# Kernel tuning notes

Measured on AMD Instinct MI355X. Metric: run time of the kernel, lower is better.

Reference implementation:

```python
import jax, jax.numpy as jnp
import numpy as np

BN_EPS = 1e-5

def _bn(x, gamma, beta, relu=True):
    # training-mode BatchNorm over all dims except channel (last)
    axes = tuple(range(x.ndim - 1))
    mu = jnp.mean(x, axes, keepdims=True)
    var = jnp.var(x, axes, keepdims=True)
    y = (x - mu) / jnp.sqrt(var + BN_EPS) * gamma + beta
    return jax.nn.relu(y) if relu else y

def _l2norm(x, eps):
    # F.normalize: x / max(||x||, eps)
    n = jnp.sqrt(jnp.sum(x * x, axis=-1, keepdims=True))
    return x / jnp.maximum(n, eps)

def setup_inputs() -> dict:
    key = jax.random.key(0)
    ks = jax.random.split(key, 16)
    B, N, H, W, C = 2, 512, 16, 32, 64
    IN_DIM = 10 + C + C + 2  # 140
    MLP3 = [128, 64]
    s = 0.02
    inp = {
        "warped_xyz": jax.random.normal(ks[0], (B, N, 3), jnp.float32),
        "warped_points": jax.random.normal(ks[1], (B, N, C), jnp.float32),
        "RF3": jax.random.normal(ks[2], (B, C, H, W), jnp.float32),
        "RF3_index": jax.random.normal(ks[3], (B, 3, H, W), jnp.float32),
        "lidar_z": jax.random.uniform(ks[4], (B, N, 1), jnp.float32),
        # conv1x1 stack (mlp3)
        "W1": jax.random.normal(ks[5], (IN_DIM, MLP3[0]), jnp.float32) * s,
        "b1": jnp.zeros((MLP3[0],), jnp.float32),
        "g1": jnp.ones((MLP3[0],), jnp.float32),
        "be1": jnp.zeros((MLP3[0],), jnp.float32),
        "W2": jax.random.normal(ks[6], (MLP3[0], MLP3[1]), jnp.float32) * s,
        "b2": jnp.zeros((MLP3[1],), jnp.float32),
        "g2": jnp.ones((MLP3[1],), jnp.float32),
        "be2": jnp.zeros((MLP3[1],), jnp.float32),
        # conv1d stack (mlp4 = [feats_dim//2], then 2 logits)
        "M1w": jax.random.normal(ks[7], (MLP3[1], MLP3[1] // 2), jnp.float32) * s,
        "M1b": jnp.zeros((MLP3[1] // 2,), jnp.float32),
        "M1g": jnp.ones((MLP3[1] // 2,), jnp.float32),
        "M1be": jnp.zeros((MLP3[1] // 2,), jnp.float32),
        "M2w": jax.random.normal(ks[8], (MLP3[1] // 2, 2), jnp.float32) * s,
        "M2b": jnp.zeros((2,), jnp.float32),
    }
    return inp

def reference(warped_xyz, warped_points, RF3, RF3_index, lidar_z,
              W1, b1, g1, be1, W2, b2, g2, be2,
              M1w, M1b, M1g, M1be, M2w, M2b):
    B, N, _ = warped_xyz.shape
    _, Ci, H, W_ = RF3.shape
    M = H * W_
    RF3_bnc = RF3.transpose(0, 2, 3, 1).reshape(B, M, Ci)          # [B,M,C]
    idx_bnc = RF3_index.transpose(0, 2, 3, 1).reshape(B, M, 3)     # [B,M,3]

    src_xyz = warped_xyz[:, :, None, :]                             # [B,N,1,3]
    dst_xyz = idx_bnc[:, None, :, :]                                # [B,1,M,3]
    euc = (src_xyz - dst_xyz)[..., :2]                              # [B,N,M,2]
    euc_norm = jnp.sqrt(euc[..., 0:1] ** 2 + euc[..., 1:2] ** 2)    # [B,N,M,1]

    xyz_z = (warped_xyz * lidar_z)[:, :, None, :]                   # [B,N,1,3]
    src_pts = warped_points[:, :, None, :]                          # [B,N,1,C]
    dst_pts = RF3_bnc[:, None, :, :]                                # [B,1,M,C]

    geom = jnp.concatenate([
        jnp.broadcast_to(xyz_z, (B, N, M, 3)),
        jnp.broadcast_to(src_pts[..., :2], (B, N, M, 2)),
        jnp.broadcast_to(dst_xyz[..., :2], (B, N, M, 2)),
        euc, euc_norm], axis=-1)                                    # [B,N,M,10]
    desc = jnp.concatenate([
        jnp.broadcast_to(src_pts, (B, N, M, Ci)),
        jnp.broadcast_to(dst_pts, (B, N, M, Ci))], axis=-1)         # [B,N,M,2C]

    # cal_sim: cosine sim between lidar feats (src) and image feats (dst)
    src_n = _l2norm(warped_points, 1e-12)
    dst_n = _l2norm(RF3_bnc, 1e-12)
    cos = jnp.einsum('bnc,bmc->bnm', src_n, dst_n)                  # [B,N,M]
    s1 = cos / (jnp.max(cos, axis=2, keepdims=True) + 1e-6)         # src->dst norm
    s2 = cos / (jnp.max(cos, axis=1, keepdims=True) + 1e-10)        # dst->src norm
    sim = jnp.stack([s1, s2], axis=-1)                              # [B,N,M,2]

    feats = jnp.concatenate([geom, desc, sim], axis=-1)             # [B,N,M,140]
    feats = _bn(jnp.einsum('bnmi,io->bnmo', feats, W1) + b1, g1, be1)
    feats = _bn(jnp.einsum('bnmi,io->bnmo', feats, W2) + b2, g2, be2)

    aw = jax.nn.softmax(jnp.max(feats, axis=-1), axis=-1)           # [B,N,M]
    att = jnp.einsum('bnm,bnmc->bnc', aw, feats)                    # [B,N,C]

    att = _bn(att @ M1w + M1b, M1g, M1be)
    logits = att @ M2w + M2b                                        # [B,N,2]
    return logits
```

## Files before the change

### kernel.cpp

```cpp
#include <hip/hip_runtime.h>
#include <hip/hip_bf16.h>

#define B_ 2
#define N_ 512
#define M_ 512
#define O1 128
#define O2 64
#define PBIG 524288.0f
#define P3   1024.0f

typedef short s8v __attribute__((ext_vector_type(8)));
typedef float f4v __attribute__((ext_vector_type(4)));

#define WS_SRCN 0
#define WS_DSTN 65536
#define WS_P0   0
#define WS_U    131072
#define WS_Z    131072
#define WS_V    262144
#define WS_DXY  393216
#define WS_COS  395264
#define WS_RMAX 919552
#define WS_ROWS 920576
#define WS_COLS 923648
#define WS_SC2P 935936
#define WS_ST2  936960
#define WS_ST3  945152
#define WS_CMAX 949248
#define WS_W2F  950272
#define WS_W9S  954368
#define WS_X2   961536
#define WS_VF   17738752

__device__ __forceinline__ unsigned short f2bf(float f){
  unsigned u = __float_as_uint(f);
  unsigned r = (u + 0x7fffu + ((u >> 16) & 1u)) >> 16;
  return (unsigned short)r;
}
__device__ __forceinline__ float bf2f(unsigned short h){
  return __uint_as_float(((unsigned)h) << 16);
}
__device__ __forceinline__ unsigned pk2(float lo, float hi){
  return (unsigned)f2bf(lo) | ((unsigned)f2bf(hi) << 16);
}
__device__ __forceinline__ unsigned pk_trunc(float lo, float hi){
  return __builtin_amdgcn_perm(__float_as_uint(hi), __float_as_uint(lo), 0x07060302u);
}
__device__ __forceinline__ f4v relu4(f4v z){
  z[0] = fmaxf(z[0], 0.f); z[1] = fmaxf(z[1], 0.f);
  z[2] = fmaxf(z[2], 0.f); z[3] = fmaxf(z[3], 0.f);
  return z;
}

__global__ __launch_bounds__(128) void k1(const float* __restrict__ wxyz,
    const float* __restrict__ wpts, const float* __restrict__ lz,
    const float* __restrict__ rf3, const float* __restrict__ rf3i,
    const float* __restrict__ W1, const float* __restrict__ W2, float* __restrict__ ws){
  int t = threadIdx.x;
  if (blockIdx.x < 1024){
    int blk = blockIdx.x; int b = blk >> 9, n = blk & 511;
    int bn = b*N_ + n;
    __shared__ float wp[64]; __shared__ float sxyz[3]; __shared__ float slz; __shared__ float srn;
    if (t < 64) wp[t] = wpts[bn*64 + t];
    if (t >= 64 && t < 67) sxyz[t-64] = wxyz[bn*3 + (t-64)];
    if (t == 67) slz = lz[bn];
    __syncthreads();
    if (t < 64){
      float v = wp[t]*wp[t];
      v += __shfl_down(v,32); v += __shfl_down(v,16); v += __shfl_down(v,8);
      v += __shfl_down(v,4);  v += __shfl_down(v,2);  v += __shfl_down(v,1);
      if (t == 0) srn = 1.0f / fmaxf(sqrtf(v), 1e-12f);
    }
    __syncthreads();
    if (t < 64) ws[WS_SRCN + bn*64 + t] = wp[t]*srn;
    int o = t;
    float x = sxyz[0], y = sxyz[1], z = sxyz[2], l = slz;
    float acc = x*l*W1[0*O1+o] + y*l*W1[1*O1+o] + z*l*W1[2*O1+o]
              + wp[0]*W1[3*O1+o] + wp[1]*W1[4*O1+o]
              + x*W1[7*O1+o] + y*W1[8*O1+o];
    #pragma unroll 8
    for (int c = 0; c < 64; ++c) acc += wp[c]*W1[(10+c)*O1+o];
    ws[WS_U + bn*O1 + o] = acc;
  } else if (blockIdx.x < 2048){
    int blk = blockIdx.x - 1024; int b = blk >> 9, m = blk & 511;
    int bm = b*M_ + m;
    __shared__ float rf[64]; __shared__ float sdx, sdy, srn2;
    if (t < 64) rf[t] = rf3[(b*64 + t)*512 + m];
    if (t == 64) sdx = rf3i[(b*3 + 0)*512 + m];
    if (t == 65) sdy = rf3i[(b*3 + 1)*512 + m];
    __syncthreads();
    if (t < 64){
      float v = rf[t]*rf[t];
      v += __shfl_down(v,32); v += __shfl_down(v,16); v += __shfl_down(v,8);
      v += __shfl_down(v,4);  v += __shfl_down(v,2);  v += __shfl_down(v,1);
      if (t == 0) srn2 = 1.0f / fmaxf(sqrtf(v), 1e-12f);
    }
    __syncthreads();
    if (t < 64) ws[WS_DSTN + bm*64 + t] = rf[t]*srn2;
    if (t == 0){ ws[WS_DXY + bm*2+0] = sdx; ws[WS_DXY + bm*2+1] = sdy; }
    int o = t;
    float acc = sdx*(W1[5*O1+o] - W1[7*O1+o]) + sdy*(W1[6*O1+o] - W1[8*O1+o]);
    #pragma unroll 8
    for (int c = 0; c < 64; ++c) acc += rf[c]*W1[(74+c)*O1+o];
    ws[WS_V + bm*O1 + o] = acc;
  } else {
    unsigned short* wf = (unsigned short*)(ws + WS_W2F);
    for (int i = t; i < 8192; i += 128){
      int j = i & 7, ll = (i >> 3) & 63, ct = (i >> 9) & 3, k0q = i >> 11;
      int oo = k0q*32 + (ll >> 4)*8 + j, c = ct*16 + (ll & 15);
      wf[i] = f2bf(W2[oo*O2 + c]);
    }
  }
}

__global__ __launch_bounds__(256) void k2(float* __restrict__ ws){
  int blk = blockIdx.x; int b = blk >> 9, n = blk & 511; int t = threadIdx.x;
  int bn = b*N_ + n;
  __shared__ __align__(16) float sn[64];
  __shared__ float dnt[64*65];
  __shared__ float part[4*64];
  if (t < 64) sn[t] = ws[WS_SRCN + bn*64 + t];
  float lmax = -3.4e38f;
  for (int chunk = 0; chunk < 8; ++chunk){
    __syncthreads();
    const float4* src = (const float4*)(ws + WS_DSTN + (size_t)(b*M_ + chunk*64)*64);
    #pragma unroll
    for (int i = 0; i < 4; ++i){
      float4 v = src[t + i*256];
      int base = (t + i*256)*4; int mm = base >> 6, c = base & 63;
      float* dp = &dnt[mm*65 + c];
      dp[0]=v.x; dp[1]=v.y; dp[2]=v.z; dp[3]=v.w;
    }
    __syncthreads();
    {
      int mm = t & 63, cg2 = t >> 6;
      const float* dr = &dnt[mm*65 + cg2*16];
      const float* sr = &sn[cg2*16];
      float p = 0.f;
      #pragma unroll
      for (int k = 0; k < 16; ++k) p += sr[k]*dr[k];
      part[cg2*64 + mm] = p;
    }
    __syncthreads();
    if (t < 64){
      float d = part[t] + part[64+t] + part[128+t] + part[192+t];
      ws[WS_COS + bn*M_ + chunk*64 + t] = d;
      lmax = fmaxf(lmax, d);
    }
  }
  if (t < 64){
    lmax = fmaxf(lmax, __shfl_xor(lmax,32)); lmax = fmaxf(lmax, __shfl_xor(lmax,16));
    lmax = fmaxf(lmax, __shfl_xor(lmax,8));  lmax = fmaxf(lmax, __shfl_xor(lmax,4));
    lmax = fmaxf(lmax, __shfl_xor(lmax,2));  lmax = fmaxf(lmax, __shfl_xor(lmax,1));
    if (t == 0) ws[WS_RMAX + bn] = 1.0f / (lmax + 1e-6f);
  }
}

__global__ __launch_bounds__(256) void k2r(const float* __restrict__ wxyz, float* __restrict__ ws){
  int blk = blockIdx.x;
  int b = blk >> 5; int c0 = (blk & 31)*16;
  int t = threadIdx.x;
  int cl = t & 15, seg = t >> 4;
  int col = c0 + cl;
  int bm = b*M_ + col;
  float dx = ws[WS_DXY + bm*2+0], dy = ws[WS_DXY + bm*2+1];
  float mx = -3.4e38f, se = 0.f, sc = 0.f, s1c = 0.f;
  for (int i = 0; i < 32; ++i){
    int bn = b*N_ + seg*32 + i;
    float cv = ws[WS_COS + (size_t)bn*M_ + col];
    float ri = ws[WS_RMAX + bn];
    float sx = wxyz[bn*3+0], sy = wxyz[bn*3+1];
    float ex = sx-dx, ey = sy-dy;
    se += sqrtf(ex*ex + ey*ey);
    mx = fmaxf(mx, cv);
    sc += cv;
    s1c += cv*ri;
  }
  __shared__ float r0[256], r1[256], r2[256], r3[256];
  r0[t]=mx; r1[t]=se; r2[t]=s1c; r3[t]=sc;
  __syncthreads();
  for (int s = 8; s > 0; s >>= 1){
    if (seg < s){
      int o2 = t + s*16;
      r0[t] = fmaxf(r0[t], r0[o2]); r1[t] += r1[o2]; r2[t] += r2[o2]; r3[t] += r3[o2];
    }
    __syncthreads();
  }
  if (t < 16){
    int bmw = b*M_ + c0 + t;
    float ci = 1.0f/(r0[t] + 1e-10f);
    ws[WS_CMAX + bmw] = ci;
    ws[WS_COLS + bmw] = r1[t];
    ws[WS_COLS + 1024 + bmw] = r2[t];
    ws[WS_COLS + 2048 + bmw] = r3[t]*ci;
  }
}

__global__ __launch_bounds__(256) void k3a(const float* __restrict__ wxyz, float* __restrict__ ws){
  int bn = blockIdx.x; int b = bn >> 9; int t = threadIdx.x;
  float ri = ws[WS_RMAX + bn];
  float sx = wxyz[bn*3+0], sy = wxyz[bn*3+1];
  float q[9];
  #pragma unroll
  for (int j = 0; j < 9; ++j) q[j] = 0.f;
  #pragma unroll
  for (int k = 0; k < 2; ++k){
    int m = t + k*256;
    float2 d = *(const float2*)(ws + WS_DXY + (size_t)(b*M_+m)*2);
    float ex = sx-d.x, ey = sy-d.y;
    float en = sqrtf(ex*ex + ey*ey);
    float cv = ws[WS_COS + (size_t)bn*M_ + m];
    float ci = ws[WS_CMAX + b*M_ + m];
    float s2 = cv*ci;
    q[0]+=en; q[1]+=cv; q[2]+=s2; q[3]+=en*en; q[4]+=cv*cv; q[5]+=s2*s2;
    q[6]+=en*cv; q[7]+=en*s2; q[8]+=cv*cv*ci;
  }
  #pragma unroll
  for (int j = 0; j < 9; ++j){
    float v = q[j];
    v += __shfl_xor(v,1); v += __shfl_xor(v,2); v += __shfl_xor(v,4);
    v += __shfl_xor(v,8); v += __shfl_xor(v,16); v += __shfl_xor(v,32);
    q[j] = v;
  }
  __shared__ float wr[9][4];
  int w = t >> 6;
  if ((t & 63) == 0){
    #pragma unroll
    for (int j = 0; j < 9; ++j) wr[j][w] = q[j];
  }
  __syncthreads();
  if (t < 9){
    float Q = wr[t][0] + wr[t][1] + wr[t][2] + wr[t][3];
    float f = (t==1 || t==6 || t==8) ? ri : ((t==4) ? ri*ri : 1.0f);
    float s = f*Q;
    if (t < 3) ws[WS_ROWS + t*1024 + bn] = s;
    atomicAdd(&ws[WS_SC2P + (bn & 63)*16 + t], s);
  }
}

__global__ __launch_bounds__(256) void k3s(const float* __restrict__ W1,
    const float* __restrict__ b1, const float* __restrict__ g1,
    const float* __restrict__ be1, float* __restrict__ ws){
  int o = blockIdx.x; int t = threadIdx.x;
  __shared__ float scal[9];
  __shared__ float wr[12][4];
  __shared__ float sA1, sC1;
  if (t < 9){
    float s = 0.f;
    #pragma unroll 8
    for (int r = 0; r < 64; ++r) s += ws[WS_SC2P + r*16 + t];
    scal[t] = s;
  }
  float b1o = b1[o];
  float uu[4], vv[4];
  float a[12];
  #pragma unroll
  for (int j = 0; j < 12; ++j) a[j] = 0.f;
  #pragma unroll
  for (int k = 0; k < 4; ++k){
    int i = t + k*256;
    float u = ws[WS_U + (size_t)i*O1 + o] + b1o;
    float v = ws[WS_V + (size_t)i*O1 + o];
    uu[k] = u; vv[k] = v;
    float ren = ws[WS_ROWS + i], rs1 = ws[WS_ROWS + 1024 + i], rs2 = ws[WS_ROWS + 2048 + i];
    float cen = ws[WS_COLS + i], cs1 = ws[WS_COLS + 1024 + i], cs2 = ws[WS_COLS + 2048 + i];
    a[0]+=u; a[1]+=u*u; a[2]+=u*ren; a[3]+=u*rs1; a[4]+=u*rs2;
    a[5]+=v; a[6]+=v*v; a[7]+=v*cen; a[8]+=v*cs1; a[9]+=v*cs2;
    if (k < 2){ a[10]+=u; a[11]+=v; }
  }
  #pragma unroll
  for (int j = 0; j < 12; ++j){
    float v = a[j];
    v += __shfl_xor(v,1); v += __shfl_xor(v,2); v += __shfl_xor(v,4);
    v += __shfl_xor(v,8); v += __shfl_xor(v,16); v += __shfl_xor(v,32);
    a[j] = v;
  }
  int w = t >> 6;
  if ((t & 63) == 0){
    #pragma unroll
    for (int j = 0; j < 12; ++j) wr[j][w] = a[j];
  }
  __syncthreads();
  if (t == 0){
    float A[12];
    #pragma unroll
    for (int j = 0; j < 12; ++j) A[j] = wr[j][0] + wr[j][1] + wr[j][2] + wr[j][3];
    float w9 = W1[9*O1+o], wa = W1[138*O1+o], wb = W1[139*O1+o];
    float S1 = 512.f*(A[0] + A[5]) + w9*scal[0] + wa*scal[1] + wb*scal[2];
    float Q1 = 512.f*(A[1] + A[6])
      + 2.f*(A[10]*A[11] + (A[0]-A[10])*(A[5]-A[11]))
      + w9*w9*scal[3] + wa*wa*scal[4] + wb*wb*scal[5]
      + 2.f*(w9*wa*scal[6] + w9*wb*scal[7] + wa*wb*scal[8])
      + 2.f*(w9*A[2] + wa*A[3] + wb*A[4])
      + 2.f*(w9*A[7] + wa*A[8] + wb*A[9]);
    float mu = S1/PBIG, var = Q1/PBIG - mu*mu;
    float istd = rsqrtf(var + 1e-5f);
    float A1v = g1[o]*istd;
    sA1 = A1v; sC1 = be1[o] - mu*A1v;
    ws[WS_W9S + o]       = w9*A1v;
    ws[WS_W9S + 128 + o] = wa*A1v;
    ws[WS_W9S + 256 + o] = wb*A1v;
  }
  __syncthreads();
  float A1 = sA1, C1 = sC1;
  int k0q = o >> 5, quad = (o >> 3) & 3, j = o & 7;
  #pragma unroll
  for (int k = 0; k < 4; ++k){
    int i = t + k*256;
    ws[WS_P0 + (size_t)i*O1 + o] = uu[k]*A1 + C1;
    int b = i >> 9, m = i & 511;
    int mc = m >> 7, w2 = (m >> 5) & 3, mt = (m >> 4) & 1, l16 = m & 15;
    ws[WS_VF + (size_t)(((b*4 + mc)*4 + w2)*4096) + k0q*1024 + mt*512 + (quad*16 + l16)*8 + j]
      = vv[k]*A1;
  }
}

__global__ __launch_bounds__(256, 4) void k4(const float* __restrict__ wxyz,
    float* __restrict__ ws){
  int blk = blockIdx.x; int bn = blk >> 2, mc = blk & 3;
  int b = bn >> 9; int t = threadIdx.x;
  __shared__ __align__(16) float p0s[128], w9s[128], was[128], wbs[128];
  __shared__ float ls[64], lq[64];
  if (t < 64){ ls[t] = 0.f; lq[t] = 0.f; }
  if (t < 128){
    p0s[t] = ws[WS_P0 + bn*O1 + t];
    w9s[t] = ws[WS_W9S + t];
    was[t] = ws[WS_W9S + 128 + t];
    wbs[t] = ws[WS_W9S + 256 + t];
  }
  __syncthreads();
  int ll = t & 63, w = t >> 6, l16 = ll & 15, quad = ll >> 4;
  float sx = wxyz[bn*3+0], sy = wxyz[bn*3+1];
  float ri = ws[WS_RMAX + bn];
  uint4* xf4 = (uint4*)(ws + WS_X2) + (size_t)bn*4096;
  const unsigned short* wBg = (const unsigned short*)(ws + WS_W2F);
  union U8 { s8v v; unsigned u[4]; };
  int mA = mc*128 + w*32 + l16, mB = mA + 16;
  float2 dA = *(const float2*)(ws + WS_DXY + (size_t)(b*M_+mA)*2);
  float2 dB = *(const float2*)(ws + WS_DXY + (size_t)(b*M_+mB)*2);
  float cvA = ws[WS_COS + (size_t)bn*M_ + mA], cvB = ws[WS_COS + (size_t)bn*M_ + mB];
  float ciA = ws[WS_CMAX + b*M_ + mA],         ciB = ws[WS_CMAX + b*M_ + mB];
  float exA = sx-dA.x, eyA = sy-dA.y; float en0 = sqrtf(exA*exA + eyA*eyA);
  float exB = sx-dB.x, eyB = sy-dB.y; float en1 = sqrtf(exB*exB + eyB*eyB);
  float s10 = cvA*ri, s20 = cvA*ciA;
  float s11 = cvB*ri, s21 = cvB*ciB;
  const float* vfb = ws + WS_VF + (size_t)(((b*4 + mc)*4 + w)*4096) + ll*8;
  f4v acc[2][4];
  #pragma unroll
  for (int i = 0; i < 2; ++i)
    #pragma unroll
    for (int j = 0; j < 4; ++j) acc[i][j] = (f4v){0.f,0.f,0.f,0.f};
  #pragma unroll
  for (int k0q = 0; k0q < 4; ++k0q){
    int ko = k0q*32 + quad*8;
    f4v p0a = *(const f4v*)&p0s[ko], p0b = *(const f4v*)&p0s[ko+4];
    f4v w9a = *(const f4v*)&w9s[ko], w9b = *(const f4v*)&w9s[ko+4];
    f4v waa = *(const f4v*)&was[ko], wab = *(const f4v*)&was[ko+4];
    f4v wba = *(const f4v*)&wbs[ko], wbb = *(const f4v*)&wbs[ko+4];
    const float* vA = vfb + k0q*1024;
    const float* vB = vA + 512;
    f4v vA0 = *(const f4v*)(vA), vA1 = *(const f4v*)(vA + 4);
    f4v vB0 = *(const f4v*)(vB), vB1 = *(const f4v*)(vB + 4);
    f4v zaA = relu4(p0a + vA0 + en0*w9a + s10*waa + s20*wba);
    f4v zbA = relu4(p0b + vA1 + en0*w9b + s10*wab + s20*wbb);
    f4v zaB = relu4(p0a + vB0 + en1*w9a + s11*waa + s21*wba);
    f4v zbB = relu4(p0b + vB1 + en1*w9b + s11*wab + s21*wbb);
    U8 uA, uB;
    uA.u[0] = pk_trunc(zaA[0], zaA[1]); uA.u[1] = pk_trunc(zaA[2], zaA[3]);
    uA.u[2] = pk_trunc(zbA[0], zbA[1]); uA.u[3] = pk_trunc(zbA[2], zbA[3]);
    uB.u[0] = pk_trunc(zaB[0], zaB[1]); uB.u[1] = pk_trunc(zaB[2], zaB[3]);
    uB.u[2] = pk_trunc(zbB[0], zbB[1]); uB.u[3] = pk_trunc(zbB[2], zbB[3]);
    #pragma unroll
    for (int ct = 0; ct < 4; ++ct){
      s8v bw = *(const s8v*)&wBg[((k0q*4 + ct)*64 + ll)*8];
      acc[0][ct] = __builtin_amdgcn_mfma_f32_16x16x32_bf16(bw, uA.v, acc[0][ct], 0,0,0);
      acc[1][ct] = __builtin_amdgcn_mfma_f32_16x16x32_bf16(bw, uB.v, acc[1][ct], 0,0,0);
    }
  }
  #pragma unroll
  for (int mt = 0; mt < 2; ++mt){
    uint4 u0, u1;
    u0.x = pk2(acc[mt][0][0], acc[mt][0][1]); u0.y = pk2(acc[mt][0][2], acc[mt][0][3]);
    u0.z = pk2(acc[mt][1][0], acc[mt][1][1]); u0.w = pk2(acc[mt][1][2], acc[mt][1][3]);
    u1.x = pk2(acc[mt][2][0], acc[mt][2][1]); u1.y = pk2(acc[mt][2][2], acc[mt][2][3]);
    u1.z = pk2(acc[mt][3][0], acc[mt][3][1]); u1.w = pk2(acc[mt][3][2], acc[mt][3][3]);
    xf4[((((mc*4 + w)*2 + mt)*2 + 0)*64) + ll] = u0;
    xf4[((((mc*4 + w)*2 + mt)*2 + 1)*64) + ll] = u1;
  }
  #pragma unroll
  for (int ct = 0; ct < 4; ++ct){
    #pragma unroll
    for (int r = 0; r < 4; ++r){
      float a0 = acc[0][ct][r], a1 = acc[1][ct][r];
      float s = a0 + a1;
      float q = a0*a0 + a1*a1;
      s += __shfl_xor(s,1); s += __shfl_xor(s,2); s += __shfl_xor(s,4); s += __shfl_xor(s,8);
      q += __shfl_xor(q,1); q += __shfl_xor(q,2); q += __shfl_xor(q,4); q += __shfl_xor(q,8);
      if (l16 == 0){
        atomicAdd(&ls[ct*16 + quad*4 + r], s);
        atomicAdd(&lq[ct*16 + quad*4 + r], q);
      }
    }
  }
  __syncthreads();
  int rep = blk & 63;
  if (t < 64) atomicAdd(&ws[WS_ST2 + rep*128 + t], ls[t]);
  else if (t < 128) atomicAdd(&ws[WS_ST2 + rep*128 + t], lq[t-64]);
}

__global__ __launch_bounds__(256) void k5(const float* __restrict__ g2,
    const float* __restrict__ be2, const float* __restrict__ M1w,
    const float* __restrict__ M1b, float* __restrict__ ws){
  int bn = blockIdx.x; int t = threadIdx.x;
  __shared__ float sa2[64], sc2[64];
  __shared__ float s_mx[512];
  __shared__ float s_aw[512];
  __shared__ float red[256];
  __shared__ float part[64*65];
  __shared__ float s_att[64];
  __shared__ float sgmax, sinvS;
  if (t < 64){
    float s = 0.f, q = 0.f;
    #pragma unroll 8
    for (int r = 0; r < 64; ++r){ s += ws[WS_ST2 + r*128 + t]; q += ws[WS_ST2 + r*128 + 64 + t]; }
    float mu = s/PBIG, var = q/PBIG - mu*mu;
    float istd = rsqrtf(var + 1e-5f);
    float A2 = g2[t]*istd;
    sa2[t] = A2; sc2[t] = be2[t] - mu*A2;
  }
  __syncthreads();
  int ll = t & 63, w = t >> 6, l16 = ll & 15, quad = ll >> 4;
  const uint4* xf4 = (const uint4*)(ws + WS_X2) + (size_t)bn*4096;
  uint4 xv[4][2][2];
  #pragma unroll
  for (int mc = 0; mc < 4; ++mc)
    #pragma unroll
    for (int mt = 0; mt < 2; ++mt)
      #pragma unroll
      for (int cp = 0; cp < 2; ++cp)
        xv[mc][mt][cp] = xf4[((((mc*4 + w)*2 + mt)*2 + cp)*64) + ll];
  float a2r[4][4], c2r[4][4];
  #pragma unroll
  for (int ct = 0; ct < 4; ++ct)
    #pragma unroll
    for (int r = 0; r < 4; ++r){
      int c = ct*16 + quad*4 + r;
      a2r[ct][r] = sa2[c]; c2r[ct][r] = sc2[c];
    }
  #pragma unroll
  for (int mc = 0; mc < 4; ++mc){
    #pragma unroll
    for (int mt = 0; mt < 2; ++mt){
      float mx = 0.f;
      #pragma unroll
      for (int cp = 0; cp < 2; ++cp){
        uint4 uv = xv[mc][mt][cp];
        int c0t = 2*cp, c1t = 2*cp + 1;
        float x0 = bf2f((unsigned short)(uv.x & 0xffffu));
        float x1 = bf2f((unsigned short)(uv.x >> 16));
        float x2 = bf2f((unsigned short)(uv.y & 0xffffu));
        float x3 = bf2f((unsigned short)(uv.y >> 16));
        float x4 = bf2f((unsigned short)(uv.z & 0xffffu));
        float x5 = bf2f((unsigned short)(uv.z >> 16));
        float x6 = bf2f((unsigned short)(uv.w & 0xffffu));
        float x7 = bf2f((unsigned short)(uv.w >> 16));
        mx = fmaxf(mx, a2r[c0t][0]*x0 + c2r[c0t][0]);
        mx = fmaxf(mx, a2r[c0t][1]*x1 + c2r[c0t][1]);
        mx = fmaxf(mx, a2r[c0t][2]*x2 + c2r[c0t][2]);
        mx = fmaxf(mx, a2r[c0t][3]*x3 + c2r[c0t][3]);
        mx = fmaxf(mx, a2r[c1t][0]*x4 + c2r[c1t][0]);
        mx = fmaxf(mx, a2r[c1t][1]*x5 + c2r[c1t][1]);
        mx = fmaxf(mx, a2r[c1t][2]*x6 + c2r[c1t][2]);
        mx = fmaxf(mx, a2r[c1t][3]*x7 + c2r[c1t][3]);
      }
      mx = fmaxf(mx, __shfl_xor(mx,16));
      mx = fmaxf(mx, __shfl_xor(mx,32));
      if (quad == 0) s_mx[mc*128 + w*32 + mt*16 + l16] = mx;
    }
  }
  __syncthreads();
  red[t] = fmaxf(s_mx[t], s_mx[t+256]);
  __syncthreads();
  for (int s = 128; s > 0; s >>= 1){ if (t < s) red[t] = fmaxf(red[t], red[t+s]); __syncthreads(); }
  if (t == 0) sgmax = red[0];
  __syncthreads();
  float e0 = expf(s_mx[t] - sgmax), e1 = expf(s_mx[t+256] - sgmax);
  s_aw[t] = e0; s_aw[t+256] = e1;
  red[t] = e0 + e1;
  __syncthreads();
  for (int s = 128; s > 0; s >>= 1){ if (t < s) red[t] += red[t+s]; __syncthreads(); }
  if (t == 0) sinvS = 1.0f / red[0];
  __syncthreads();
  float acc[4][4];
  #pragma unroll
  for (int ct = 0; ct < 4; ++ct)
    #pragma unroll
    for (int r = 0; r < 4; ++r) acc[ct][r] = 0.f;
  #pragma unroll
  for (int mc = 0; mc < 4; ++mc){
    #pragma unroll
    for (int mt = 0; mt < 2; ++mt){
      float aw = s_aw[mc*128 + w*32 + mt*16 + l16];
      #pragma unroll
      for (int cp = 0; cp < 2; ++cp){
        uint4 uv = xv[mc][mt][cp];
        int c0t = 2*cp, c1t = 2*cp + 1;
        float x0 = bf2f((unsigned short)(uv.x & 0xffffu));
        float x1 = bf2f((unsigned short)(uv.x >> 16));
        float x2 = bf2f((unsigned short)(uv.y & 0xffffu));
        float x3 = bf2f((unsigned short)(uv.y >> 16));
        float x4 = bf2f((unsigned short)(uv.z & 0xffffu));
        float x5 = bf2f((unsigned short)(uv.z >> 16));
        float x6 = bf2f((unsigned short)(uv.w & 0xffffu));
        float x7 = bf2f((unsigned short)(uv.w >> 16));
        acc[c0t][0] += aw*fmaxf(a2r[c0t][0]*x0 + c2r[c0t][0], 0.f);
        acc[c0t][1] += aw*fmaxf(a2r[c0t][1]*x1 + c2r[c0t][1], 0.f);
        acc[c0t][2] += aw*fmaxf(a2r[c0t][2]*x2 + c2r[c0t][2], 0.f);
        acc[c0t][3] += aw*fmaxf(a2r[c0t][3]*x3 + c2r[c0t][3], 0.f);
        acc[c1t][0] += aw*fmaxf(a2r[c1t][0]*x4 + c2r[c1t][0], 0.f);
        acc[c1t][1] += aw*fmaxf(a2r[c1t][1]*x5 + c2r[c1t][1], 0.f);
        acc[c1t][2] += aw*fmaxf(a2r[c1t][2]*x6 + c2r[c1t][2], 0.f);
        acc[c1t][3] += aw*fmaxf(a2r[c1t][3]*x7 + c2r[c1t][3], 0.f);
      }
    }
  }
  int row = w*16 + l16;
  #pragma unroll
  for (int ct = 0; ct < 4; ++ct)
    #pragma unroll
    for (int r = 0; r < 4; ++r)
      part[row*65 + ct*16 + quad*4 + r] = acc[ct][r];
  __syncthreads();
  if (t < 64){
    float a = 0.f;
    #pragma unroll 8
    for (int r = 0; r < 64; ++r) a += part[r*65 + t];
    s_att[t] = a * sinvS;
  }
  __syncthreads();
  if (t < 32){
    float z = M1b[t];
    #pragma unroll 8
    for (int c = 0; c < 64; ++c) z += s_att[c]*M1w[c*32 + t];
    ws[WS_Z + bn*32 + t] = z;
    int rep = bn & 63;
    atomicAdd(&ws[WS_ST3 + rep*64 + t], z);
    atomicAdd(&ws[WS_ST3 + rep*64 + 32 + t], z*z);
  }
}

__global__ __launch_bounds__(256) void k6(const float* __restrict__ M1g,
    const float* __restrict__ M1be, const float* __restrict__ M2w,
    const float* __restrict__ M2b, const float* __restrict__ ws, float* __restrict__ out){
  int t = threadIdx.x; int s = blockIdx.x*256 + t;
  __shared__ float sa3[32], sc3[32];
  if (t < 32){
    float su = 0.f, q = 0.f;
    #pragma unroll 8
    for (int r = 0; r < 64; ++r){ su += ws[WS_ST3 + r*64 + t]; q += ws[WS_ST3 + r*64 + 32 + t]; }
    float mu = su/P3, var = q/P3 - mu*mu;
    float istd = rsqrtf(var + 1e-5f);
    float A3 = M1g[t]*istd;
    sa3[t] = A3; sc3[t] = M1be[t] - mu*A3;
  }
  __syncthreads();
  float a0 = M2b[0], a1 = M2b[1];
  #pragma unroll
  for (int j = 0; j < 32; ++j){
    float y = fmaxf(ws[WS_Z + s*32 + j]*sa3[j] + sc3[j], 0.f);
    a0 += y*M2w[j*2+0]; a1 += y*M2w[j*2+1];
  }
  out[s*2+0] = a0; out[s*2+1] = a1;
}

extern "C" void kernel_launch(void* const* d_in, const int* in_sizes, int n_in,
                              void* d_out, int out_size, void* d_ws, size_t ws_size,
                              hipStream_t stream){
  const float* wxyz = (const float*)d_in[0];
  const float* wpts = (const float*)d_in[1];
  const float* rf3  = (const float*)d_in[2];
  const float* rf3i = (const float*)d_in[3];
  const float* lz   = (const float*)d_in[4];
  const float* W1   = (const float*)d_in[5];
  const float* b1   = (const float*)d_in[6];
  const float* g1   = (const float*)d_in[7];
  const float* be1  = (const float*)d_in[8];
  const float* W2   = (const float*)d_in[9];
  const float* g2   = (const float*)d_in[11];
  const float* be2  = (const float*)d_in[12];
  const float* M1w  = (const float*)d_in[13];
  const float* M1b  = (const float*)d_in[14];
  const float* M1g  = (const float*)d_in[15];
  const float* M1be = (const float*)d_in[16];
  const float* M2w  = (const float*)d_in[17];
  const float* M2b  = (const float*)d_in[18];
  float* ws  = (float*)d_ws;
  float* out = (float*)d_out;
  hipMemsetAsync(ws + WS_SC2P, 0, 13312*sizeof(float), stream);
  k1 <<<2049,128,0,stream>>>(wxyz, wpts, lz, rf3, rf3i, W1, W2, ws);
  k2 <<<1024,256,0,stream>>>(ws);
  k2r<<<64,256,0,stream>>>(wxyz, ws);
  k3a<<<1024,256,0,stream>>>(wxyz, ws);
  k3s<<<128,256,0,stream>>>(W1, b1, g1, be1, ws);
  k4 <<<4096,256,0,stream>>>(wxyz, ws);
  k5 <<<1024,256,0,stream>>>(g2, be2, M1w, M1b, ws);
  k6 <<<4,256,0,stream>>>(M1g, M1be, M2w, M2b, ws, out);
}
```

Before: 214.8 us.

## Split BN1 stats kernel, move V relayout into k2, fold scaling into k4

Replaces the 128-block k3s with a 256-block partial-sum kernel that accumulates per-channel stats into replicated atomics, plus a single-block finalizer. The V re-layout moves into extra blocks of k2, and the workspace memset moves into extra blocks of k2r, which removes the memset launch. k4 now computes p0 and the A1 scaling of V on the fly from U, and k5's softmax reductions use wave shuffles instead of tree reductions in shared memory. The aim is to fix k3s's low parallelism and redundant passes, at the cost of one extra launch and more arithmetic in k4.

```diff
diff --git a/kernel.cpp b/kernel.cpp
--- a/kernel.cpp
+++ b/kernel.cpp
@@ -14,7 +14,7 @@
 
 #define WS_SRCN 0
 #define WS_DSTN 65536
-#define WS_P0   0
+#define WS_APART 65536
 #define WS_U    131072
 #define WS_Z    131072
 #define WS_V    262144
@@ -23,6 +23,7 @@
 #define WS_RMAX 919552
 #define WS_ROWS 920576
 #define WS_COLS 923648
+#define WS_A1C  926720
 #define WS_SC2P 935936
 #define WS_ST2  936960
 #define WS_ST3  945152
@@ -114,7 +115,20 @@
 }
 
 __global__ __launch_bounds__(256) void k2(float* __restrict__ ws){
-  int blk = blockIdx.x; int b = blk >> 9, n = blk & 511; int t = threadIdx.x;
+  int blk = blockIdx.x; int t = threadIdx.x;
+  if (blk >= 1024){
+    int q = blk - 1024; int vb = q >> 4, mc = (q >> 2) & 3, w2 = q & 3;
+    float* dst = ws + WS_VF + (size_t)(((vb*4 + mc)*4 + w2)*4096);
+    const float* Vsrc = ws + WS_V + (size_t)vb*512*O1;
+    for (int p = t; p < 4096; p += 256){
+      int k0q = p >> 10, r = p & 1023, mt = r >> 9, r2 = r & 511, qr = r2 >> 3, j = r2 & 7;
+      int o = k0q*32 + (qr >> 4)*8 + j;
+      int m = mc*128 + w2*32 + mt*16 + (qr & 15);
+      dst[p] = Vsrc[(size_t)m*O1 + o];
+    }
+    return;
+  }
+  int b = blk >> 9, n = blk & 511;
   int bn = b*N_ + n;
   __shared__ __align__(16) float sn[64];
   __shared__ float dnt[64*65];
@@ -157,9 +171,16 @@
 }
 
 __global__ __launch_bounds__(256) void k2r(const float* __restrict__ wxyz, float* __restrict__ ws){
-  int blk = blockIdx.x;
+  int blk = blockIdx.x; int t = threadIdx.x;
+  if (blk >= 64){
+    int zb = blk - 64;
+    for (int i = zb*256 + t; i < 62464; i += 6*256){
+      if (i < 13312) ws[WS_SC2P + i] = 0.f;
+      else ws[WS_APART + (i - 13312)] = 0.f;
+    }
+    return;
+  }
   int b = blk >> 5; int c0 = (blk & 31)*16;
-  int t = threadIdx.x;
   int cl = t & 15, seg = t >> 4;
   int col = c0 + cl;
   int bm = b*M_ + col;
@@ -238,92 +259,83 @@
   }
 }
 
-__global__ __launch_bounds__(256) void k3s(const float* __restrict__ W1,
-    const float* __restrict__ b1, const float* __restrict__ g1,
-    const float* __restrict__ be1, float* __restrict__ ws){
-  int o = blockIdx.x; int t = threadIdx.x;
-  __shared__ float scal[9];
-  __shared__ float wr[12][4];
-  __shared__ float sA1, sC1;
-  if (t < 9){
-    float s = 0.f;
-    #pragma unroll 8
-    for (int r = 0; r < 64; ++r) s += ws[WS_SC2P + r*16 + t];
-    scal[t] = s;
-  }
+__global__ __launch_bounds__(256) void k3sA(const float* __restrict__ b1, float* __restrict__ ws){
+  int blk = blockIdx.x; int t = threadIdx.x;
+  int o = t & 127, pair = t >> 7;
   float b1o = b1[o];
-  float uu[4], vv[4];
   float a[12];
   #pragma unroll
   for (int j = 0; j < 12; ++j) a[j] = 0.f;
   #pragma unroll
-  for (int k = 0; k < 4; ++k){
-    int i = t + k*256;
+  for (int k = 0; k < 2; ++k){
+    int i = blk*4 + pair*2 + k;
     float u = ws[WS_U + (size_t)i*O1 + o] + b1o;
     float v = ws[WS_V + (size_t)i*O1 + o];
-    uu[k] = u; vv[k] = v;
     float ren = ws[WS_ROWS + i], rs1 = ws[WS_ROWS + 1024 + i], rs2 = ws[WS_ROWS + 2048 + i];
     float cen = ws[WS_COLS + i], cs1 = ws[WS_COLS + 1024 + i], cs2 = ws[WS_COLS + 2048 + i];
     a[0]+=u; a[1]+=u*u; a[2]+=u*ren; a[3]+=u*rs1; a[4]+=u*rs2;
     a[5]+=v; a[6]+=v*v; a[7]+=v*cen; a[8]+=v*cs1; a[9]+=v*cs2;
-    if (k < 2){ a[10]+=u; a[11]+=v; }
-  }
+    if (i < 512){ a[10]+=u; a[11]+=v; }
+  }
+  __shared__ float apar[2][12][128];
+  #pragma unroll
+  for (int j = 0; j < 12; ++j) apar[pair][j][o] = a[j];
+  __syncthreads();
+  int rep = blk & 31;
+  for (int idx = t; idx < 1536; idx += 256){
+    int j = idx >> 7, oo = idx & 127;
+    atomicAdd(&ws[WS_APART + rep*1536 + idx], apar[0][j][oo] + apar[1][j][oo]);
+  }
+}
+
+__global__ __launch_bounds__(128) void k3sB(const float* __restrict__ W1,
+    const float* __restrict__ g1, const float* __restrict__ be1, float* __restrict__ ws){
+  int t = threadIdx.x; int o = t;
+  __shared__ float scal[9];
+  if (t < 9){
+    float s = 0.f;
+    #pragma unroll 8
+    for (int r = 0; r < 64; ++r) s += ws[WS_SC2P + r*16 + t];
+    scal[t] = s;
+  }
+  float A[12];
   #pragma unroll
   for (int j = 0; j < 12; ++j){
-    float v = a[j];
-    v += __shfl_xor(v,1); v += __shfl_xor(v,2); v += __shfl_xor(v,4);
-    v += __shfl_xor(v,8); v += __shfl_xor(v,16); v += __shfl_xor(v,32);
-    a[j] = v;
-  }
-  int w = t >> 6;
-  if ((t & 63) == 0){
-    #pragma unroll
-    for (int j = 0; j < 12; ++j) wr[j][w] = a[j];
-  }
-  __syncthreads();
-  if (t == 0){
-    float A[12];
-    #pragma unroll
-    for (int j = 0; j < 12; ++j) A[j] = wr[j][0] + wr[j][1] + wr[j][2] + wr[j][3];
-    float w9 = W1[9*O1+o], wa = W1[138*O1+o], wb = W1[139*O1+o];
-    float S1 = 512.f*(A[0] + A[5]) + w9*scal[0] + wa*scal[1] + wb*scal[2];
-    float Q1 = 512.f*(A[1] + A[6])
-      + 2.f*(A[10]*A[11] + (A[0]-A[10])*(A[5]-A[11]))
-      + w9*w9*scal[3] + wa*wa*scal[4] + wb*wb*scal[5]
-      + 2.f*(w9*wa*scal[6] + w9*wb*scal[7] + wa*wb*scal[8])
-      + 2.f*(w9*A[2] + wa*A[3] + wb*A[4])
-      + 2.f*(w9*A[7] + wa*A[8] + wb*A[9]);
-    float mu = S1/PBIG, var = Q1/PBIG - mu*mu;
-    float istd = rsqrtf(var + 1e-5f);
-    float A1v = g1[o]*istd;
-    sA1 = A1v; sC1 = be1[o] - mu*A1v;
-    ws[WS_W9S + o]       = w9*A1v;
-    ws[WS_W9S + 128 + o] = wa*A1v;
-    ws[WS_W9S + 256 + o] = wb*A1v;
-  }
-  __syncthreads();
-  float A1 = sA1, C1 = sC1;
-  int k0q = o >> 5, quad = (o >> 3) & 3, j = o & 7;
-  #pragma unroll
-  for (int k = 0; k < 4; ++k){
-    int i = t + k*256;
-    ws[WS_P0 + (size_t)i*O1 + o] = uu[k]*A1 + C1;
-    int b = i >> 9, m = i & 511;
-    int mc = m >> 7, w2 = (m >> 5) & 3, mt = (m >> 4) & 1, l16 = m & 15;
-    ws[WS_VF + (size_t)(((b*4 + mc)*4 + w2)*4096) + k0q*1024 + mt*512 + (quad*16 + l16)*8 + j]
-      = vv[k]*A1;
-  }
+    float s = 0.f;
+    #pragma unroll 8
+    for (int r = 0; r < 32; ++r) s += ws[WS_APART + r*1536 + j*128 + o];
+    A[j] = s;
+  }
+  __syncthreads();
+  float w9 = W1[9*O1+o], wa = W1[138*O1+o], wb = W1[139*O1+o];
+  float S1 = 512.f*(A[0] + A[5]) + w9*scal[0] + wa*scal[1] + wb*scal[2];
+  float Q1 = 512.f*(A[1] + A[6])
+    + 2.f*(A[10]*A[11] + (A[0]-A[10])*(A[5]-A[11]))
+    + w9*w9*scal[3] + wa*wa*scal[4] + wb*wb*scal[5]
+    + 2.f*(w9*wa*scal[6] + w9*wb*scal[7] + wa*wb*scal[8])
+    + 2.f*(w9*A[2] + wa*A[3] + wb*A[4])
+    + 2.f*(w9*A[7] + wa*A[8] + wb*A[9]);
+  float mu = S1/PBIG, var = Q1/PBIG - mu*mu;
+  float istd = rsqrtf(var + 1e-5f);
+  float A1v = g1[o]*istd;
+  ws[WS_A1C + o] = A1v;
+  ws[WS_A1C + 128 + o] = be1[o] - mu*A1v;
+  ws[WS_W9S + o]       = w9*A1v;
+  ws[WS_W9S + 128 + o] = wa*A1v;
+  ws[WS_W9S + 256 + o] = wb*A1v;
 }
 
 __global__ __launch_bounds__(256, 4) void k4(const float* __restrict__ wxyz,
-    float* __restrict__ ws){
+    const float* __restrict__ b1, float* __restrict__ ws){
   int blk = blockIdx.x; int bn = blk >> 2, mc = blk & 3;
   int b = bn >> 9; int t = threadIdx.x;
-  __shared__ __align__(16) float p0s[128], w9s[128], was[128], wbs[128];
+  __shared__ __align__(16) float p0s[128], a1s[128], w9s[128], was[128], wbs[128];
   __shared__ float ls[64], lq[64];
   if (t < 64){ ls[t] = 0.f; lq[t] = 0.f; }
   if (t < 128){
-    p0s[t] = ws[WS_P0 + bn*O1 + t];
+    float A1 = ws[WS_A1C + t], C1 = ws[WS_A1C + 128 + t];
+    p0s[t] = (ws[WS_U + bn*O1 + t] + b1[t])*A1 + C1;
+    a1s[t] = A1;
     w9s[t] = ws[WS_W9S + t];
     was[t] = ws[WS_W9S + 128 + t];
     wbs[t] = ws[WS_W9S + 256 + t];
@@ -354,6 +366,7 @@
   for (int k0q = 0; k0q < 4; ++k0q){
     int ko = k0q*32 + quad*8;
     f4v p0a = *(const f4v*)&p0s[ko], p0b = *(const f4v*)&p0s[ko+4];
+    f4v a1a = *(const f4v*)&a1s[ko], a1b = *(const f4v*)&a1s[ko+4];
     f4v w9a = *(const f4v*)&w9s[ko], w9b = *(const f4v*)&w9s[ko+4];
     f4v waa = *(const f4v*)&was[ko], wab = *(const f4v*)&was[ko+4];
     f4v wba = *(const f4v*)&wbs[ko], wbb = *(const f4v*)&wbs[ko+4];
@@ -361,10 +374,10 @@
     const float* vB = vA + 512;
     f4v vA0 = *(const f4v*)(vA), vA1 = *(const f4v*)(vA + 4);
     f4v vB0 = *(const f4v*)(vB), vB1 = *(const f4v*)(vB + 4);
-    f4v zaA = relu4(p0a + vA0 + en0*w9a + s10*waa + s20*wba);
-    f4v zbA = relu4(p0b + vA1 + en0*w9b + s10*wab + s20*wbb);
-    f4v zaB = relu4(p0a + vB0 + en1*w9a + s11*waa + s21*wba);
-    f4v zbB = relu4(p0b + vB1 + en1*w9b + s11*wab + s21*wbb);
+    f4v zaA = relu4(p0a + vA0*a1a + en0*w9a + s10*waa + s20*wba);
+    f4v zbA = relu4(p0b + vA1*a1b + en0*w9b + s10*wab + s20*wbb);
+    f4v zaB = relu4(p0a + vB0*a1a + en1*w9a + s11*waa + s21*wba);
+    f4v zbB = relu4(p0b + vB1*a1b + en1*w9b + s11*wab + s21*wbb);
     U8 uA, uB;
     uA.u[0] = pk_trunc(zaA[0], zaA[1]); uA.u[1] = pk_trunc(zaA[2], zaA[3]);
     uA.u[2] = pk_trunc(zbA[0], zbA[1]); uA.u[3] = pk_trunc(zbA[2], zbA[3]);
@@ -415,10 +428,9 @@
   __shared__ float sa2[64], sc2[64];
   __shared__ float s_mx[512];
   __shared__ float s_aw[512];
-  __shared__ float red[256];
+  __shared__ float wred[4], wred2[4];
   __shared__ float part[64*65];
   __shared__ float s_att[64];
-  __shared__ float sgmax, sinvS;
   if (t < 64){
     float s = 0.f, q = 0.f;
     #pragma unroll 8
@@ -479,18 +491,26 @@
     }
   }
   __syncthreads();
-  red[t] = fmaxf(s_mx[t], s_mx[t+256]);
-  __syncthreads();
-  for (int s = 128; s > 0; s >>= 1){ if (t < s) red[t] = fmaxf(red[t], red[t+s]); __syncthreads(); }
-  if (t == 0) sgmax = red[0];
-  __syncthreads();
-  float e0 = expf(s_mx[t] - sgmax), e1 = expf(s_mx[t+256] - sgmax);
+  {
+    float v = fmaxf(s_mx[t], s_mx[t+256]);
+    v = fmaxf(v, __shfl_xor(v,1));  v = fmaxf(v, __shfl_xor(v,2));
+    v = fmaxf(v, __shfl_xor(v,4));  v = fmaxf(v, __shfl_xor(v,8));
+    v = fmaxf(v, __shfl_xor(v,16)); v = fmaxf(v, __shfl_xor(v,32));
+    if (ll == 0) wred[w] = v;
+  }
+  __syncthreads();
+  float gmax = fmaxf(fmaxf(wred[0], wred[1]), fmaxf(wred[2], wred[3]));
+  float e0 = expf(s_mx[t] - gmax), e1 = expf(s_mx[t+256] - gmax);
   s_aw[t] = e0; s_aw[t+256] = e1;
-  red[t] = e0 + e1;
-  __syncthreads();
-  for (int s = 128; s > 0; s >>= 1){ if (t < s) red[t] += red[t+s]; __syncthreads(); }
-  if (t == 0) sinvS = 1.0f / red[0];
-  __syncthreads();
+  {
+    float sv = e0 + e1;
+    sv += __shfl_xor(sv,1);  sv += __shfl_xor(sv,2);
+    sv += __shfl_xor(sv,4);  sv += __shfl_xor(sv,8);
+    sv += __shfl_xor(sv,16); sv += __shfl_xor(sv,32);
+    if (ll == 0) wred2[w] = sv;
+  }
+  __syncthreads();
+  float sinv = 1.0f / (wred2[0] + wred2[1] + wred2[2] + wred2[3]);
   float acc[4][4];
   #pragma unroll
   for (int ct = 0; ct < 4; ++ct)
@@ -535,7 +555,7 @@
     float a = 0.f;
     #pragma unroll 8
     for (int r = 0; r < 64; ++r) a += part[r*65 + t];
-    s_att[t] = a * sinvS;
+    s_att[t] = a * sinv;
   }
   __syncthreads();
   if (t < 32){
@@ -596,13 +616,13 @@
   const float* M2b  = (const float*)d_in[18];
   float* ws  = (float*)d_ws;
   float* out = (float*)d_out;
-  hipMemsetAsync(ws + WS_SC2P, 0, 13312*sizeof(float), stream);
-  k1 <<<2049,128,0,stream>>>(wxyz, wpts, lz, rf3, rf3i, W1, W2, ws);
-  k2 <<<1024,256,0,stream>>>(ws);
-  k2r<<<64,256,0,stream>>>(wxyz, ws);
-  k3a<<<1024,256,0,stream>>>(wxyz, ws);
-  k3s<<<128,256,0,stream>>>(W1, b1, g1, be1, ws);
-  k4 <<<4096,256,0,stream>>>(wxyz, ws);
-  k5 <<<1024,256,0,stream>>>(g2, be2, M1w, M1b, ws);
-  k6 <<<4,256,0,stream>>>(M1g, M1be, M2w, M2b, ws, out);
-}
+  k1  <<<2049,128,0,stream>>>(wxyz, wpts, lz, rf3, rf3i, W1, W2, ws);
+  k2  <<<1056,256,0,stream>>>(ws);
+  k2r <<<70,256,0,stream>>>(wxyz, ws);
+  k3a <<<1024,256,0,stream>>>(wxyz, ws);
+  k3sA<<<256,256,0,stream>>>(b1, ws);
+  k3sB<<<1,128,0,stream>>>(W1, g1, be1, ws);
+  k4  <<<4096,256,0,stream>>>(wxyz, b1, ws);
+  k5  <<<1024,256,0,stream>>>(g2, be2, M1w, M1b, ws);
+  k6  <<<4,256,0,stream>>>(M1g, M1be, M2w, M2b, ws, out);
+}
```

New measurement: 239.4 us. 1.11x slower.

## Split column reduction across more blocks with atomics and stage W2 in LDS

Applied to the files above, without the earlier changes.

The column-reduction kernel k2r now splits the N dimension into 8 row slices, launching 512 blocks instead of 64. Partial max and sums are combined through global atomics, with the max using an order-preserving integer encoding. A small finalize kernel then inverts the max and scales the third column sum. Separately, k4 copies the bf16 W2 fragment into shared memory once per block instead of reading it from global memory inside the MFMA loop. This adds an extra launch, a second memset and 16KB of LDS per block, which may reduce k4 occupancy.

```diff
diff --git a/kernel.cpp b/kernel.cpp
--- a/kernel.cpp
+++ b/kernel.cpp
@@ -46,6 +46,14 @@
 __device__ __forceinline__ unsigned pk_trunc(float lo, float hi){
   return __builtin_amdgcn_perm(__float_as_uint(hi), __float_as_uint(lo), 0x07060302u);
 }
+__device__ __forceinline__ unsigned fenc(float f){
+  unsigned b = __float_as_uint(f);
+  return (b & 0x80000000u) ? ~b : (b | 0x80000000u);
+}
+__device__ __forceinline__ float fdec(unsigned u){
+  unsigned b = (u & 0x80000000u) ? (u & 0x7fffffffu) : ~u;
+  return __uint_as_float(b);
+}
 __device__ __forceinline__ f4v relu4(f4v z){
   z[0] = fmaxf(z[0], 0.f); z[1] = fmaxf(z[1], 0.f);
   z[2] = fmaxf(z[2], 0.f); z[3] = fmaxf(z[3], 0.f);
@@ -158,15 +166,17 @@
 
 __global__ __launch_bounds__(256) void k2r(const float* __restrict__ wxyz, float* __restrict__ ws){
   int blk = blockIdx.x;
-  int b = blk >> 5; int c0 = (blk & 31)*16;
+  int rs = blk & 7; int cg = (blk >> 3) & 31; int b = blk >> 8;
+  int c0 = cg*16;
   int t = threadIdx.x;
   int cl = t & 15, seg = t >> 4;
   int col = c0 + cl;
   int bm = b*M_ + col;
   float dx = ws[WS_DXY + bm*2+0], dy = ws[WS_DXY + bm*2+1];
   float mx = -3.4e38f, se = 0.f, sc = 0.f, s1c = 0.f;
-  for (int i = 0; i < 32; ++i){
-    int bn = b*N_ + seg*32 + i;
+  #pragma unroll
+  for (int i = 0; i < 4; ++i){
+    int bn = b*N_ + rs*64 + seg*4 + i;
     float cv = ws[WS_COS + (size_t)bn*M_ + col];
     float ri = ws[WS_RMAX + bn];
     float sx = wxyz[bn*3+0], sy = wxyz[bn*3+1];
@@ -188,12 +198,19 @@
   }
   if (t < 16){
     int bmw = b*M_ + c0 + t;
-    float ci = 1.0f/(r0[t] + 1e-10f);
-    ws[WS_CMAX + bmw] = ci;
-    ws[WS_COLS + bmw] = r1[t];
-    ws[WS_COLS + 1024 + bmw] = r2[t];
-    ws[WS_COLS + 2048 + bmw] = r3[t]*ci;
-  }
+    atomicMax((unsigned*)ws + WS_CMAX + bmw, fenc(r0[t]));
+    atomicAdd(&ws[WS_COLS + bmw], r1[t]);
+    atomicAdd(&ws[WS_COLS + 1024 + bmw], r2[t]);
+    atomicAdd(&ws[WS_COLS + 2048 + bmw], r3[t]);
+  }
+}
+
+__global__ __launch_bounds__(256) void k2f(float* __restrict__ ws){
+  int bm = blockIdx.x*256 + threadIdx.x;
+  unsigned e = ((unsigned*)ws)[WS_CMAX + bm];
+  float ci = 1.0f / (fdec(e) + 1e-10f);
+  ws[WS_CMAX + bm] = ci;
+  ws[WS_COLS + 2048 + bm] *= ci;
 }
 
 __global__ __launch_bounds__(256) void k3a(const float* __restrict__ wxyz, float* __restrict__ ws){
@@ -319,8 +336,15 @@
     float* __restrict__ ws){
   int blk = blockIdx.x; int bn = blk >> 2, mc = blk & 3;
   int b = bn >> 9; int t = threadIdx.x;
+  __shared__ __align__(16) unsigned short wBf[8192];
   __shared__ __align__(16) float p0s[128], w9s[128], was[128], wbs[128];
   __shared__ float ls[64], lq[64];
+  {
+    const s8v* g = (const s8v*)(ws + WS_W2F);
+    s8v* l = (s8v*)wBf;
+    #pragma unroll
+    for (int c2 = 0; c2 < 4; ++c2) l[c2*256 + t] = g[c2*256 + t];
+  }
   if (t < 64){ ls[t] = 0.f; lq[t] = 0.f; }
   if (t < 128){
     p0s[t] = ws[WS_P0 + bn*O1 + t];
@@ -333,7 +357,6 @@
   float sx = wxyz[bn*3+0], sy = wxyz[bn*3+1];
   float ri = ws[WS_RMAX + bn];
   uint4* xf4 = (uint4*)(ws + WS_X2) + (size_t)bn*4096;
-  const unsigned short* wBg = (const unsigned short*)(ws + WS_W2F);
   union U8 { s8v v; unsigned u[4]; };
   int mA = mc*128 + w*32 + l16, mB = mA + 16;
   float2 dA = *(const float2*)(ws + WS_DXY + (size_t)(b*M_+mA)*2);
@@ -372,7 +395,7 @@
     uB.u[2] = pk_trunc(zbB[0], zbB[1]); uB.u[3] = pk_trunc(zbB[2], zbB[3]);
     #pragma unroll
     for (int ct = 0; ct < 4; ++ct){
-      s8v bw = *(const s8v*)&wBg[((k0q*4 + ct)*64 + ll)*8];
+      s8v bw = *(const s8v*)&wBf[((k0q*4 + ct)*64 + ll)*8];
       acc[0][ct] = __builtin_amdgcn_mfma_f32_16x16x32_bf16(bw, uA.v, acc[0][ct], 0,0,0);
       acc[1][ct] = __builtin_amdgcn_mfma_f32_16x16x32_bf16(bw, uB.v, acc[1][ct], 0,0,0);
     }
@@ -596,10 +619,12 @@
   const float* M2b  = (const float*)d_in[18];
   float* ws  = (float*)d_ws;
   float* out = (float*)d_out;
-  hipMemsetAsync(ws + WS_SC2P, 0, 13312*sizeof(float), stream);
+  hipMemsetAsync(ws + WS_SC2P, 0, 14336*sizeof(float), stream);
+  hipMemsetAsync(ws + WS_COLS, 0, 3072*sizeof(float), stream);
   k1 <<<2049,128,0,stream>>>(wxyz, wpts, lz, rf3, rf3i, W1, W2, ws);
   k2 <<<1024,256,0,stream>>>(ws);
-  k2r<<<64,256,0,stream>>>(wxyz, ws);
+  k2r<<<512,256,0,stream>>>(wxyz, ws);
+  k2f<<<4,256,0,stream>>>(ws);
   k3a<<<1024,256,0,stream>>>(wxyz, ws);
   k3s<<<128,256,0,stream>>>(W1, b1, g1, be1, ws);
   k4 <<<4096,256,0,stream>>>(wxyz, ws);
```

Result: no change. 215.0 us (+0.1%).
